# Optimization experiments

Measured on AMD Instinct MI355X. Metric: run time of the kernel, lower is better.

## Reference

```python
import jax, jax.numpy as jnp
import numpy as np

B, S, HID = 1, 4096, 2048
H, KV, D = 16, 8, 128
N_REP = H // KV
SCALING = float(128 ** -0.5)   # query_pre_attn_scalar ** -0.5
SOFTCAP = 50.0
WINDOW = 1024
NEG = -1e9


def setup_inputs() -> dict:
    key = jax.random.key(0)
    ks = jax.random.split(key, 6)
    hidden_states = jax.random.normal(ks[0], (B, S, HID), dtype=jnp.float32)
    Wq = jax.random.normal(ks[1], (HID, H * D), dtype=jnp.float32) * 0.02
    Wk = jax.random.normal(ks[2], (HID, KV * D), dtype=jnp.float32) * 0.02
    Wv = jax.random.normal(ks[3], (HID, KV * D), dtype=jnp.float32) * 0.02
    Wo = jax.random.normal(ks[4], (H * D, HID), dtype=jnp.float32) * 0.02
    # RoPE tables [1, S, D]
    inv_freq = 1.0 / (10000.0 ** (jnp.arange(0, D, 2, dtype=jnp.float32) / D))
    freqs = jnp.outer(jnp.arange(S, dtype=jnp.float32), inv_freq)   # [S, D/2]
    emb = jnp.concatenate([freqs, freqs], axis=-1)                  # [S, D]
    cos = jnp.cos(emb)[None]
    sin = jnp.sin(emb)[None]
    # causal + sliding-window additive mask [1, 1, S, S]
    i = jnp.arange(S)[:, None]
    j = jnp.arange(S)[None, :]
    allowed = (j <= i) & ((i - j) < WINDOW)
    attention_mask = jnp.where(allowed, 0.0, NEG).astype(jnp.float32)[None, None]
    return {"hidden_states": hidden_states, "cos": cos, "sin": sin,
            "attention_mask": attention_mask, "Wq": Wq, "Wk": Wk, "Wv": Wv, "Wo": Wo}


def _rotate_half(x):
    x1, x2 = jnp.split(x, 2, axis=-1)
    return jnp.concatenate([-x2, x1], axis=-1)


def reference(hidden_states, cos, sin, attention_mask, Wq, Wk, Wv, Wo):
    b, s, _ = hidden_states.shape
    # projections -> [B, heads, S, D]
    q = (hidden_states @ Wq).reshape(b, s, H, D).transpose(0, 2, 1, 3)
    k = (hidden_states @ Wk).reshape(b, s, KV, D).transpose(0, 2, 1, 3)
    v = (hidden_states @ Wv).reshape(b, s, KV, D).transpose(0, 2, 1, 3)
    # RoPE (unsqueeze_dim=1)
    c = cos[:, None]  # [B, 1, S, D]
    sn = sin[:, None]
    q = q * c + _rotate_half(q) * sn
    k = k * c + _rotate_half(k) * sn
    # repeat_kv (GQA)
    k = jnp.repeat(k, N_REP, axis=1)
    v = jnp.repeat(v, N_REP, axis=1)
    # scores with softcap + mask
    scores = jnp.einsum('bhqd,bhkd->bhqk', q, k) * SCALING
    scores = jnp.tanh(scores / SOFTCAP) * SOFTCAP
    scores = scores + attention_mask
    attn = jax.nn.softmax(scores.astype(jnp.float32), axis=-1).astype(q.dtype)
    out = jnp.einsum('bhqk,bhkd->bhqd', attn, v)
    out = out.transpose(0, 2, 1, 3).reshape(b, s, H * D)
    return out @ Wo
```

## Files before the change

### kernel.cpp

```cpp
#include <hip/hip_runtime.h>

#define S 4096
#define HID 2048
#define NH 16
#define NKV 8
#define HD 128
#define WINDOW 1024
#define SCALING 0.08838834764831845f
#define SOFTCAP 50.0f

typedef __bf16 bf16x8 __attribute__((ext_vector_type(8)));
typedef __bf16 bf16x4 __attribute__((ext_vector_type(4)));
typedef float f32x4 __attribute__((ext_vector_type(4)));

__device__ inline void gll16(const void* g, void* l) {
  __builtin_amdgcn_global_load_lds((const __attribute__((address_space(1))) void*)g,
                                   (__attribute__((address_space(3))) void*)l, 16, 0, 0);
}

__global__ void cvt_hs(const float* __restrict__ in, __bf16* __restrict__ out, int n4) {
  int i = blockIdx.x * blockDim.x + threadIdx.x;
  if (i < n4) {
    float4 v = ((const float4*)in)[i];
    bf16x4 o;
    o[0] = (__bf16)v.x; o[1] = (__bf16)v.y; o[2] = (__bf16)v.z; o[3] = (__bf16)v.w;
    ((bf16x4*)out)[i] = o;
  }
}

__global__ void transpose_w(const float* __restrict__ in, __bf16* __restrict__ out, int K, int N) {
  __shared__ float tile[64][65];
  int k0 = blockIdx.x * 64, n0 = blockIdx.y * 64;
  int t = threadIdx.x;
#pragma unroll
  for (int e = 0; e < 16; ++e) {
    int f = e * 256 + t; int r = f >> 6, c = f & 63;
    tile[r][c] = in[(size_t)(k0 + r) * N + n0 + c];
  }
  __syncthreads();
#pragma unroll
  for (int e = 0; e < 16; ++e) {
    int f = e * 256 + t; int r = f >> 6, c = f & 63;
    out[(size_t)(n0 + r) * K + k0 + c] = (__bf16)tile[c][r];
  }
}

__global__ void vtrans(const __bf16* __restrict__ qkv, __bf16* __restrict__ vt) {
  __shared__ float tile[64][65];
  int s0 = blockIdx.x * 64, d0 = blockIdx.y * 64;
  int t = threadIdx.x;
#pragma unroll
  for (int e = 0; e < 16; ++e) {
    int f = e * 256 + t; int r = f >> 6, c = f & 63;
    tile[r][c] = (float)qkv[(size_t)(s0 + r) * 4096 + 3072 + d0 + c];
  }
  __syncthreads();
#pragma unroll
  for (int e = 0; e < 16; ++e) {
    int f = e * 256 + t; int r = f >> 6, c = f & 63;
    vt[(size_t)(d0 + r) * S + s0 + c] = (__bf16)tile[c][r];
  }
}

__global__ void rope_qk(const __bf16* __restrict__ qkv, const float* __restrict__ cosp,
                        const float* __restrict__ sinp, __bf16* __restrict__ qr,
                        __bf16* __restrict__ kr) {
  int t = blockIdx.x * 256 + threadIdx.x;
  int d = t & 63;
  int h = (t >> 6) % 24;
  int s = t / (64 * 24);
  float c = cosp[(size_t)s * 128 + d];
  float sn = sinp[(size_t)s * 128 + d];
  if (h < NH) {
    const __bf16* src = qkv + (size_t)s * 4096 + h * 128;
    float x1 = (float)src[d], x2 = (float)src[d + 64];
    __bf16* dst = qr + ((size_t)h * S + s) * 128;
    dst[d] = (__bf16)(x1 * c - x2 * sn);
    dst[d + 64] = (__bf16)(x2 * c + x1 * sn);
  } else {
    int kv = h - NH;
    const __bf16* src = qkv + (size_t)s * 4096 + 2048 + kv * 128;
    float x1 = (float)src[d], x2 = (float)src[d + 64];
    __bf16* dst = kr + ((size_t)kv * S + s) * 128;
    dst[d] = (__bf16)(x1 * c - x2 * sn);
    dst[d + 64] = (__bf16)(x2 * c + x1 * sn);
  }
}

template <typename OutT>
__global__ __launch_bounds__(256) void gemm_bt(const __bf16* __restrict__ A,
                                               const __bf16* __restrict__ B,
                                               OutT* __restrict__ C, int N, int K) {
  __shared__ __align__(16) __bf16 As[128 * 64];
  __shared__ __align__(16) __bf16 Bs[128 * 64];
  int m0 = blockIdx.x * 128, n0 = blockIdx.y * 128;
  int t = threadIdx.x;
  int lane = t & 63, wave = t >> 6;
  int wm = wave & 1, wn = wave >> 1;
  int quad = lane >> 4, l16 = lane & 15;

  f32x4 acc[4][4] = {};

  const __bf16* Abase = A + (size_t)m0 * K;
  const __bf16* Bbase = B + (size_t)n0 * K;

  for (int kk = 0; kk < K; kk += 64) {
    __syncthreads();
#pragma unroll
    for (int i = 0; i < 4; ++i) {
      int off = (i * 256 + t) * 8;
      int row = off >> 6, col = off & 63;
      gll16(Abase + (size_t)row * K + kk + col, &As[off]);
      gll16(Bbase + (size_t)row * K + kk + col, &Bs[off]);
    }
    __syncthreads();
#pragma unroll
    for (int ks = 0; ks < 64; ks += 32) {
      bf16x8 af[4], bfr[4];
#pragma unroll
      for (int i = 0; i < 4; ++i)
        af[i] = *(const bf16x8*)&As[(wm * 64 + i * 16 + l16) * 64 + ks + quad * 8];
#pragma unroll
      for (int j = 0; j < 4; ++j)
        bfr[j] = *(const bf16x8*)&Bs[(wn * 64 + j * 16 + l16) * 64 + ks + quad * 8];
#pragma unroll
      for (int i = 0; i < 4; ++i)
#pragma unroll
        for (int j = 0; j < 4; ++j)
          acc[i][j] = __builtin_amdgcn_mfma_f32_16x16x32_bf16(af[i], bfr[j], acc[i][j], 0, 0, 0);
    }
  }
#pragma unroll
  for (int i = 0; i < 4; ++i)
#pragma unroll
    for (int j = 0; j < 4; ++j)
#pragma unroll
      for (int r = 0; r < 4; ++r) {
        int row = m0 + wm * 64 + i * 16 + quad * 4 + r;
        int col = n0 + wn * 64 + j * 16 + l16;
        C[(size_t)row * N + col] = (OutT)acc[i][j][r];
      }
}

__global__ __launch_bounds__(512) void attn(const __bf16* __restrict__ qr,
                                            const __bf16* __restrict__ kr,
                                            const __bf16* __restrict__ vt,
                                            __bf16* __restrict__ ao) {
  __shared__ __align__(16) __bf16 Ks[64 * 128];
  __shared__ __align__(16) __bf16 Vs[128 * 64];
  __shared__ __align__(16) __bf16 Ps[8][2][16 * 72];

  int q0 = blockIdx.x * 128;
  int kvh = blockIdx.y;
  int t = threadIdx.x, lane = t & 63, wave = t >> 6;
  int quad = lane >> 4, l16 = lane & 15;
  int h = kvh * 2 + (wave & 1);
  int qbase = q0 + (wave >> 1) * 32;

  bf16x8 qf[2][4];
#pragma unroll
  for (int mi = 0; mi < 2; ++mi) {
    const __bf16* qptr = qr + ((size_t)h * S + qbase + mi * 16 + l16) * 128;
#pragma unroll
    for (int ks = 0; ks < 4; ++ks)
      qf[mi][ks] = *(const bf16x8*)&qptr[ks * 32 + quad * 8];
  }

  f32x4 o[2][8] = {};
  float lpart[2][4] = {};

  int lo = q0 - (WINDOW - 1); if (lo < 0) lo = 0;
  int kt_begin = (lo / 64) * 64;
  int kt_end = q0 + 128;

  const __bf16* kbase0 = kr + (size_t)kvh * S * 128;
  const __bf16* vbase0 = vt + (size_t)kvh * 128 * S;

  float4 kreg[2], vreg[2];
  {
    const __bf16* kb = kbase0 + (size_t)kt_begin * 128;
    const __bf16* vb = vbase0 + kt_begin;
#pragma unroll
    for (int i = 0; i < 2; ++i) {
      int off = i * 512 + t;
      kreg[i] = *(const float4*)(kb + (size_t)off * 8);
      vreg[i] = *(const float4*)(vb + (size_t)(off >> 3) * S + (off & 7) * 8);
    }
  }

  const float XS = SCALING / SOFTCAP;

  for (int kt0 = kt_begin; kt0 < kt_end; kt0 += 64) {
    __syncthreads();
#pragma unroll
    for (int i = 0; i < 2; ++i) {
      int off = i * 512 + t;
      { int r = off >> 4, c = off & 15;
        *(float4*)&Ks[r * 128 + ((c ^ (r & 15)) * 8)] = kreg[i]; }
      { int r = off >> 3, c = off & 7;
        *(float4*)&Vs[r * 64 + ((c ^ (r & 7)) * 8)] = vreg[i]; }
    }
    __syncthreads();

    if (kt0 + 64 < kt_end) {
      const __bf16* kb = kbase0 + (size_t)(kt0 + 64) * 128;
      const __bf16* vb = vbase0 + (kt0 + 64);
#pragma unroll
      for (int i = 0; i < 2; ++i) {
        int off = i * 512 + t;
        kreg[i] = *(const float4*)(kb + (size_t)off * 8);
        vreg[i] = *(const float4*)(vb + (size_t)(off >> 3) * S + (off & 7) * 8);
      }
    }

    if (kt0 > qbase + 31 || kt0 + 63 < qbase - (WINDOW - 1)) continue;

    f32x4 sacc[2][4] = {};
#pragma unroll
    for (int nt = 0; nt < 4; ++nt) {
#pragma unroll
      for (int ks = 0; ks < 4; ++ks) {
        bf16x8 b = *(const bf16x8*)&Ks[(nt * 16 + l16) * 128 + (((ks * 4 + quad) ^ l16) * 8)];
        sacc[0][nt] = __builtin_amdgcn_mfma_f32_16x16x32_bf16(qf[0][ks], b, sacc[0][nt], 0, 0, 0);
        sacc[1][nt] = __builtin_amdgcn_mfma_f32_16x16x32_bf16(qf[1][ks], b, sacc[1][nt], 0, 0, 0);
      }
    }

    bool interior = (kt0 + 63 <= qbase) && (kt0 >= qbase - (WINDOW - 1) + 63 - 63) && (kt0 >= qbase + 31 - (WINDOW - 1));
    interior = (kt0 + 63 <= qbase) && (kt0 >= qbase + 31 - (WINDOW - 1));
    if (interior) {
#pragma unroll
      for (int mi = 0; mi < 2; ++mi)
#pragma unroll
        for (int nt = 0; nt < 4; ++nt)
#pragma unroll
          for (int r = 0; r < 4; ++r) {
            float x = sacc[mi][nt][r] * XS;
            x = fminf(fmaxf(x, -0.25f), 0.25f);
            float x2 = x * x;
            float th = x * fmaf(x2, fmaf(x2, 0.13333333f, -0.33333333f), 1.0f);
            float p = __builtin_amdgcn_exp2f(fmaf(th, 72.134752f, -72.134752f));
            lpart[mi][r] += p;
            Ps[wave][mi][(quad * 4 + r) * 72 + nt * 16 + l16] = (__bf16)p;
          }
    } else {
#pragma unroll
      for (int mi = 0; mi < 2; ++mi)
#pragma unroll
        for (int nt = 0; nt < 4; ++nt) {
          int j = kt0 + nt * 16 + l16;
#pragma unroll
          for (int r = 0; r < 4; ++r) {
            int irow = qbase + mi * 16 + quad * 4 + r;
            float x = sacc[mi][nt][r] * XS;
            x = fminf(fmaxf(x, -0.25f), 0.25f);
            float x2 = x * x;
            float th = x * fmaf(x2, fmaf(x2, 0.13333333f, -0.33333333f), 1.0f);
            float p = __builtin_amdgcn_exp2f(fmaf(th, 72.134752f, -72.134752f));
            bool ok = (j <= irow) && (irow - j < WINDOW);
            p = ok ? p : 0.0f;
            lpart[mi][r] += p;
            Ps[wave][mi][(quad * 4 + r) * 72 + nt * 16 + l16] = (__bf16)p;
          }
        }
    }

    bf16x8 pf[2][2];
#pragma unroll
    for (int mi = 0; mi < 2; ++mi)
#pragma unroll
      for (int ks = 0; ks < 2; ++ks)
        pf[mi][ks] = *(const bf16x8*)&Ps[wave][mi][l16 * 72 + ks * 32 + quad * 8];
#pragma unroll
    for (int dt = 0; dt < 8; ++dt) {
#pragma unroll
      for (int ks = 0; ks < 2; ++ks) {
        bf16x8 v = *(const bf16x8*)&Vs[(dt * 16 + l16) * 64 + (((ks * 4 + quad) ^ (l16 & 7)) * 8)];
        o[0][dt] = __builtin_amdgcn_mfma_f32_16x16x32_bf16(pf[0][ks], v, o[0][dt], 0, 0, 0);
        o[1][dt] = __builtin_amdgcn_mfma_f32_16x16x32_bf16(pf[1][ks], v, o[1][dt], 0, 0, 0);
      }
    }
  }

#pragma unroll
  for (int mi = 0; mi < 2; ++mi)
#pragma unroll
    for (int r = 0; r < 4; ++r) {
      float ls = lpart[mi][r];
#pragma unroll
      for (int x = 1; x < 16; x <<= 1) ls += __shfl_xor(ls, x);
      float inv = 1.f / ls;
      int row = qbase + mi * 16 + quad * 4 + r;
      __bf16* dst = ao + (size_t)row * (NH * HD) + h * HD;
#pragma unroll
      for (int dt = 0; dt < 8; ++dt)
        dst[dt * 16 + l16] = (__bf16)(o[mi][dt][r] * inv);
    }
}

extern "C" void kernel_launch(void* const* d_in, const int* in_sizes, int n_in,
                              void* d_out, int out_size, void* d_ws, size_t ws_size,
                              hipStream_t stream) {
  const float* hs   = (const float*)d_in[0];
  const float* cosp = (const float*)d_in[1];
  const float* sinp = (const float*)d_in[2];
  const float* Wq = (const float*)d_in[4];
  const float* Wk = (const float*)d_in[5];
  const float* Wv = (const float*)d_in[6];
  const float* Wo = (const float*)d_in[7];
  float* out = (float*)d_out;

  char* w = (char*)d_ws;
  __bf16* hsb   = (__bf16*)w; w += (size_t)S * HID * 2;
  __bf16* wqkvT = (__bf16*)w; w += (size_t)4096 * 2048 * 2;
  __bf16* woT   = (__bf16*)w; w += (size_t)2048 * 2048 * 2;
  __bf16* qkv   = (__bf16*)w; w += (size_t)S * 4096 * 2;
  __bf16* qr    = (__bf16*)w; w += (size_t)NH * S * HD * 2;
  __bf16* kr    = (__bf16*)w; w += (size_t)NKV * S * HD * 2;
  __bf16* vtb   = (__bf16*)w; w += (size_t)NKV * HD * S * 2;
  __bf16* ao    = (__bf16*)w; w += (size_t)S * 2048 * 2;

  cvt_hs<<<(S * HID / 4 + 255) / 256, 256, 0, stream>>>(hs, hsb, S * HID / 4);
  transpose_w<<<dim3(32, 32), 256, 0, stream>>>(Wq, wqkvT, 2048, 2048);
  transpose_w<<<dim3(32, 16), 256, 0, stream>>>(Wk, wqkvT + (size_t)2048 * 2048, 2048, 1024);
  transpose_w<<<dim3(32, 16), 256, 0, stream>>>(Wv, wqkvT + (size_t)3072 * 2048, 2048, 1024);
  transpose_w<<<dim3(32, 32), 256, 0, stream>>>(Wo, woT, 2048, 2048);

  gemm_bt<__bf16><<<dim3(32, 32), 256, 0, stream>>>(hsb, wqkvT, qkv, 4096, 2048);

  rope_qk<<<(S * 24 * 64) / 256, 256, 0, stream>>>(qkv, cosp, sinp, qr, kr);
  vtrans<<<dim3(64, 16), 256, 0, stream>>>(qkv, vtb);

  attn<<<dim3(32, NKV), 512, 0, stream>>>(qr, kr, vtb, ao);

  gemm_bt<float><<<dim3(32, 16), 256, 0, stream>>>(ao, woT, out, 2048, 2048);
}
```

Measured before the change: 423.9 us.

## Fuse RoPE into QKV GEMM epilogue and merge weight transposes into one kernel

```diff
diff --git a/kernel.cpp b/kernel.cpp
--- a/kernel.cpp
+++ b/kernel.cpp
@@ -28,31 +28,45 @@
   }
 }
 
-__global__ void transpose_w(const float* __restrict__ in, __bf16* __restrict__ out, int K, int N) {
+__global__ void prep_w(const float* __restrict__ Wq, const float* __restrict__ Wk,
+                       const float* __restrict__ Wv, const float* __restrict__ Wo,
+                       __bf16* __restrict__ wqkvT, __bf16* __restrict__ woT) {
   __shared__ float tile[64][65];
-  int k0 = blockIdx.x * 64, n0 = blockIdx.y * 64;
+  int k0 = blockIdx.x * 64;
+  int y = blockIdx.y;
+  const float* src; __bf16* dst; int Nsrc, c0, perm, n0;
+  if (y < 32)      { src = Wq; dst = wqkvT; Nsrc = 2048; c0 = y * 64;        perm = 1; n0 = y * 64; }
+  else if (y < 48) { src = Wk; dst = wqkvT; Nsrc = 1024; c0 = (y - 32) * 64; perm = 1; n0 = 2048 + (y - 32) * 64; }
+  else if (y < 64) { src = Wv; dst = wqkvT; Nsrc = 1024; c0 = (y - 48) * 64; perm = 0; n0 = 3072 + (y - 48) * 64; }
+  else             { src = Wo; dst = woT;   Nsrc = 2048; c0 = (y - 64) * 64; perm = 0; n0 = (y - 64) * 64; }
   int t = threadIdx.x;
 #pragma unroll
   for (int e = 0; e < 16; ++e) {
     int f = e * 256 + t; int r = f >> 6, c = f & 63;
-    tile[r][c] = in[(size_t)(k0 + r) * N + n0 + c];
+    tile[r][c] = src[(size_t)(k0 + r) * Nsrc + c0 + c];
   }
   __syncthreads();
 #pragma unroll
   for (int e = 0; e < 16; ++e) {
     int f = e * 256 + t; int r = f >> 6, c = f & 63;
-    out[(size_t)(n0 + r) * K + k0 + c] = (__bf16)tile[c][r];
-  }
-}
-
-__global__ void vtrans(const __bf16* __restrict__ qkv, __bf16* __restrict__ vt) {
+    int n = n0 + r;
+    if (perm) {
+      int d = n & 127, o = d >> 4;
+      int g = (o < 4) ? (o * 2) : ((o - 4) * 2 + 1);
+      n = (n & ~127) | (g << 4) | (d & 15);
+    }
+    dst[(size_t)n * 2048 + k0 + c] = (__bf16)tile[c][r];
+  }
+}
+
+__global__ void vtrans(const __bf16* __restrict__ vbuf, __bf16* __restrict__ vt) {
   __shared__ float tile[64][65];
   int s0 = blockIdx.x * 64, d0 = blockIdx.y * 64;
   int t = threadIdx.x;
 #pragma unroll
   for (int e = 0; e < 16; ++e) {
     int f = e * 256 + t; int r = f >> 6, c = f & 63;
-    tile[r][c] = (float)qkv[(size_t)(s0 + r) * 4096 + 3072 + d0 + c];
+    tile[r][c] = (float)vbuf[(size_t)(s0 + r) * 1024 + d0 + c];
   }
   __syncthreads();
 #pragma unroll
@@ -62,28 +76,84 @@
   }
 }
 
-__global__ void rope_qk(const __bf16* __restrict__ qkv, const float* __restrict__ cosp,
-                        const float* __restrict__ sinp, __bf16* __restrict__ qr,
-                        __bf16* __restrict__ kr) {
-  int t = blockIdx.x * 256 + threadIdx.x;
-  int d = t & 63;
-  int h = (t >> 6) % 24;
-  int s = t / (64 * 24);
-  float c = cosp[(size_t)s * 128 + d];
-  float sn = sinp[(size_t)s * 128 + d];
-  if (h < NH) {
-    const __bf16* src = qkv + (size_t)s * 4096 + h * 128;
-    float x1 = (float)src[d], x2 = (float)src[d + 64];
-    __bf16* dst = qr + ((size_t)h * S + s) * 128;
-    dst[d] = (__bf16)(x1 * c - x2 * sn);
-    dst[d + 64] = (__bf16)(x2 * c + x1 * sn);
+__global__ __launch_bounds__(256) void gemm_qkv(const __bf16* __restrict__ A,
+                                                const __bf16* __restrict__ B,
+                                                __bf16* __restrict__ qr,
+                                                __bf16* __restrict__ kr,
+                                                __bf16* __restrict__ vbuf,
+                                                const float* __restrict__ cosp,
+                                                const float* __restrict__ sinp) {
+  __shared__ __align__(16) __bf16 As[128 * 64];
+  __shared__ __align__(16) __bf16 Bs[128 * 64];
+  const int K = 2048;
+  int m0 = blockIdx.x * 128, n0 = blockIdx.y * 128;
+  int t = threadIdx.x;
+  int lane = t & 63, wave = t >> 6;
+  int wm = wave & 1, wn = wave >> 1;
+  int quad = lane >> 4, l16 = lane & 15;
+
+  f32x4 acc[4][4] = {};
+
+  const __bf16* Abase = A + (size_t)m0 * K;
+  const __bf16* Bbase = B + (size_t)n0 * K;
+
+  for (int kk = 0; kk < K; kk += 64) {
+    __syncthreads();
+#pragma unroll
+    for (int i = 0; i < 4; ++i) {
+      int off = (i * 256 + t) * 8;
+      int row = off >> 6, col = off & 63;
+      gll16(Abase + (size_t)row * K + kk + col, &As[off]);
+      gll16(Bbase + (size_t)row * K + kk + col, &Bs[off]);
+    }
+    __syncthreads();
+#pragma unroll
+    for (int ks = 0; ks < 64; ks += 32) {
+      bf16x8 af[4], bfr[4];
+#pragma unroll
+      for (int i = 0; i < 4; ++i)
+        af[i] = *(const bf16x8*)&As[(wm * 64 + i * 16 + l16) * 64 + ks + quad * 8];
+#pragma unroll
+      for (int j = 0; j < 4; ++j)
+        bfr[j] = *(const bf16x8*)&Bs[(wn * 64 + j * 16 + l16) * 64 + ks + quad * 8];
+#pragma unroll
+      for (int i = 0; i < 4; ++i)
+#pragma unroll
+        for (int j = 0; j < 4; ++j)
+          acc[i][j] = __builtin_amdgcn_mfma_f32_16x16x32_bf16(af[i], bfr[j], acc[i][j], 0, 0, 0);
+    }
+  }
+
+  if (n0 < 3072) {
+    __bf16* dst = (n0 < 2048) ? (qr + (size_t)(n0 >> 7) * S * 128)
+                              : (kr + (size_t)((n0 - 2048) >> 7) * S * 128);
+#pragma unroll
+    for (int i = 0; i < 4; ++i)
+#pragma unroll
+      for (int r = 0; r < 4; ++r) {
+        int row = m0 + wm * 64 + i * 16 + quad * 4 + r;
+#pragma unroll
+        for (int jp = 0; jp < 2; ++jp) {
+          int ifr = (wn * 2 + jp) * 16 + l16;
+          float c = cosp[(size_t)row * 128 + ifr];
+          float sn = sinp[(size_t)row * 128 + ifr];
+          float lo = acc[i][2 * jp][r], hi = acc[i][2 * jp + 1][r];
+          dst[(size_t)row * 128 + wn * 64 + jp * 32 + l16]      = (__bf16)(lo * c - hi * sn);
+          dst[(size_t)row * 128 + wn * 64 + jp * 32 + 16 + l16] = (__bf16)(hi * c + lo * sn);
+        }
+      }
   } else {
-    int kv = h - NH;
-    const __bf16* src = qkv + (size_t)s * 4096 + 2048 + kv * 128;
-    float x1 = (float)src[d], x2 = (float)src[d + 64];
-    __bf16* dst = kr + ((size_t)kv * S + s) * 128;
-    dst[d] = (__bf16)(x1 * c - x2 * sn);
-    dst[d + 64] = (__bf16)(x2 * c + x1 * sn);
+    int vc0 = n0 - 3072;
+#pragma unroll
+    for (int i = 0; i < 4; ++i)
+#pragma unroll
+      for (int j = 0; j < 4; ++j)
+#pragma unroll
+        for (int r = 0; r < 4; ++r) {
+          int row = m0 + wm * 64 + i * 16 + quad * 4 + r;
+          int col = vc0 + wn * 64 + j * 16 + l16;
+          vbuf[(size_t)row * 1024 + col] = (__bf16)acc[i][j][r];
+        }
   }
 }
 
@@ -226,8 +296,7 @@
       }
     }
 
-    bool interior = (kt0 + 63 <= qbase) && (kt0 >= qbase - (WINDOW - 1) + 63 - 63) && (kt0 >= qbase + 31 - (WINDOW - 1));
-    interior = (kt0 + 63 <= qbase) && (kt0 >= qbase + 31 - (WINDOW - 1));
+    bool interior = (kt0 + 63 <= qbase) && (kt0 >= qbase + 31 - (WINDOW - 1));
     if (interior) {
 #pragma unroll
       for (int mi = 0; mi < 2; ++mi)
@@ -314,22 +383,18 @@
   __bf16* hsb   = (__bf16*)w; w += (size_t)S * HID * 2;
   __bf16* wqkvT = (__bf16*)w; w += (size_t)4096 * 2048 * 2;
   __bf16* woT   = (__bf16*)w; w += (size_t)2048 * 2048 * 2;
-  __bf16* qkv   = (__bf16*)w; w += (size_t)S * 4096 * 2;
+  __bf16* vbuf  = (__bf16*)w; w += (size_t)S * 1024 * 2;
   __bf16* qr    = (__bf16*)w; w += (size_t)NH * S * HD * 2;
   __bf16* kr    = (__bf16*)w; w += (size_t)NKV * S * HD * 2;
   __bf16* vtb   = (__bf16*)w; w += (size_t)NKV * HD * S * 2;
   __bf16* ao    = (__bf16*)w; w += (size_t)S * 2048 * 2;
 
   cvt_hs<<<(S * HID / 4 + 255) / 256, 256, 0, stream>>>(hs, hsb, S * HID / 4);
-  transpose_w<<<dim3(32, 32), 256, 0, stream>>>(Wq, wqkvT, 2048, 2048);
-  transpose_w<<<dim3(32, 16), 256, 0, stream>>>(Wk, wqkvT + (size_t)2048 * 2048, 2048, 1024);
-  transpose_w<<<dim3(32, 16), 256, 0, stream>>>(Wv, wqkvT + (size_t)3072 * 2048, 2048, 1024);
-  transpose_w<<<dim3(32, 32), 256, 0, stream>>>(Wo, woT, 2048, 2048);
-
-  gemm_bt<__bf16><<<dim3(32, 32), 256, 0, stream>>>(hsb, wqkvT, qkv, 4096, 2048);
-
-  rope_qk<<<(S * 24 * 64) / 256, 256, 0, stream>>>(qkv, cosp, sinp, qr, kr);
-  vtrans<<<dim3(64, 16), 256, 0, stream>>>(qkv, vtb);
+  prep_w<<<dim3(32, 96), 256, 0, stream>>>(Wq, Wk, Wv, Wo, wqkvT, woT);
+
+  gemm_qkv<<<dim3(32, 32), 256, 0, stream>>>(hsb, wqkvT, qr, kr, vbuf, cosp, sinp);
+
+  vtrans<<<dim3(64, 16), 256, 0, stream>>>(vbuf, vtb);
 
   attn<<<dim3(32, NKV), 512, 0, stream>>>(qr, kr, vtb, ao);
 
```

Result: faster. 404.9 us (-4.5%).
